# Performance work log

Measured on AMD Instinct MI355X. Metric: run time of the kernel, lower is better.

The kernel has to match this reference:

```python
import jax, jax.numpy as jnp
import numpy as np

K = 5  # box-blur width along disparity axis

def _blur_disparity(x):
    # depthwise conv1d with ones(K)/K kernel, zero 'same' padding, along axis 1
    N, D, H, W = x.shape
    xp = jnp.pad(x, ((0, 0), (K // 2, K // 2), (0, 0), (0, 0)))
    acc = xp[:, 0:D]
    for s in range(1, K):
        acc = acc + xp[:, s:s + D]
    return acc / K

def _modal_mask(x):
    N, D, H, W = x.shape
    index = jnp.argmax(x, axis=1, keepdims=True)                 # [N,1,H,W] int
    d = jnp.arange(D, dtype=x.dtype).reshape(1, D, 1, 1)
    d2 = jnp.arange(D + 1, dtype=x.dtype).reshape(1, D + 1, 1, 1)
    ones = jnp.ones((N, 1, H, W), dtype=x.dtype)
    x_diff_r = jnp.diff(x, axis=1, prepend=ones, append=ones)    # [N,D+1,H,W]
    x_diff_l = jnp.diff(x, axis=1, prepend=ones)                 # [N,D,H,W]
    # right edge of dominant mode: first positive diff strictly right of peak
    ind_r = ((x_diff_r * (d2 > index)) > 0).astype(jnp.int32)
    index_r = jnp.argmax(ind_r, axis=1, keepdims=True) - 1
    # left edge: last negative diff at/left of peak
    ind_l = ((x_diff_l * (d <= index)) < 0).astype(jnp.int32)
    index_l = D - 1 - jnp.argmax(jnp.flip(ind_l, axis=1), axis=1, keepdims=True)
    mask1 = (d >= index_l) & (d <= index_r)
    r = jnp.minimum(index_r - index, index - index_l)
    mask2 = (d >= index - r) & (d <= index + r)
    valid = jnp.abs(2 * index - index_r - index_l) < 3           # near-symmetric mode
    return jnp.where(valid, mask1, mask2)                        # bool [N,D,H,W]

def setup_inputs() -> dict:
    key = jax.random.key(0)
    N, D, H, W = 2, 192, 256, 512
    x = jax.random.uniform(key, (N, D, H, W), dtype=jnp.float32)
    return {"x": x}

def reference(x) -> jnp.ndarray:
    N, D, H, W = x.shape
    disp = jnp.arange(D, dtype=x.dtype).reshape(1, D, 1, 1)
    x_blur = _blur_disparity(x)
    mask = _modal_mask(x_blur)
    y = x * mask                       # primary mode mass
    z = x - y
    x_blur2 = x_blur * (~mask)
    z = z * _modal_mask(x_blur2)       # secondary mode mass
    valid = (jnp.sum(y, axis=1) >= jnp.sum(z, axis=1)).astype(jnp.float32)[:, None]
    xm = valid * y + (1.0 - valid) * z
    xm = xm / jnp.sum(xm, axis=1, keepdims=True)
    out = jnp.sum(xm * disp, axis=1, keepdims=True)  # [N,1,H,W]
    return out
```

## Files before the change

kernel.cpp:

```cpp
#include <hip/hip_runtime.h>
#include <math.h>

namespace {
constexpr int D     = 192;
constexpr int HW    = 256 * 512;
constexpr int TOTAL = 2 * HW;

__device__ __forceinline__ float div5(float s) {
    const float c = 0.2f;
    float q = s * c;
    float r = __builtin_fmaf(-5.0f, q, s);
    return __builtin_fmaf(r, c, q);
}

__device__ __forceinline__ bool in_range(int d, int lo, unsigned width) {
    return (unsigned)(d - lo) <= width;
}

struct Machine {
    float bprev, maxv;
    int   index, last_fall, index_l, index_r;
    bool  r_found;

    __device__ __forceinline__ void init() {
        bprev = 1.0f;
        maxv  = -INFINITY;
        index = 0; last_fall = 0; index_l = 0;
        index_r = D - 1;
        r_found = false;
    }

    __device__ __forceinline__ void step(int d, float b) {
        float diff = b - bprev;
        bool fall  = diff < 0.0f;
        last_fall  = fall ? d : last_fall;
        bool am    = b > maxv;
        maxv       = am ? b : maxv;
        index      = am ? d : index;
        index_l    = am ? last_fall : index_l;
        bool rise  = (diff > 0.0f) & (!r_found) & (!am);
        index_r    = am ? (D - 1) : (rise ? (d - 1) : index_r);
        r_found    = am ? false : (r_found | rise);
        bprev      = b;
    }

    __device__ __forceinline__ void finish(int& lo, unsigned& wd) const {
        int r = min(index_r - index, index - index_l);
        int t = 2 * index - index_r - index_l;
        bool valid = (t > -3) && (t < 3);
        lo = valid ? index_l : (index - r);
        int hi = valid ? index_r : (index + r);
        wd = (unsigned)(hi - lo);
    }
};

template<int OFS>
__device__ __forceinline__ void loadc(const float* __restrict__ col, int c,
                                      float (&buf)[8]) {
    #pragma unroll
    for (int j = 0; j < 8; ++j)
        buf[j] = col[(size_t)(8 * c + OFS + j) * HW];
}
template<int OFS>
__device__ __forceinline__ void loadc_guard(const float* __restrict__ col, int c,
                                            float (&buf)[8]) {
    #pragma unroll
    for (int j = 0; j < 8; ++j) {
        int idx = 8 * c + OFS + j;
        buf[j] = (idx < D) ? col[(size_t)idx * HW] : 0.0f;
    }
}

template<int OFS, typename F>
__device__ __forceinline__ void stream24(const float* __restrict__ col, F&& f) {
    float A[8], B[8], C[8];
    loadc<OFS>(col, 0, A);
    loadc<OFS>(col, 1, B);
    loadc<OFS>(col, 2, C);
    int d = 0;
    auto comp = [&](float (&buf)[8]) {
        #pragma unroll
        for (int j = 0; j < 8; ++j) { f(d, buf[j]); ++d; }
    };
    for (int g = 0; g < 6; ++g) {
        comp(A); loadc<OFS>(col, 3 * g + 3, A);
        comp(B); loadc<OFS>(col, 3 * g + 4, B);
        comp(C); loadc<OFS>(col, 3 * g + 5, C);
    }
    comp(A); loadc<OFS>(col, 21, A);
    comp(B); loadc<OFS>(col, 22, B);
    comp(C);
    if (OFS == 2) loadc_guard<OFS>(col, 23, C);
    else          loadc<OFS>(col, 23, C);
    comp(A); comp(B); comp(C);
}
}

extern "C" __global__ void __launch_bounds__(256, 4)
dme_kernel(const float* __restrict__ x, float* __restrict__ out)
{
    const int n  = blockIdx.x >> 9;
    const int hw = ((blockIdx.x & 511) << 8) | threadIdx.x;
    const float* __restrict__ col = x + (size_t)n * (size_t)(D * HW) + hw;

    const float x0 = col[0];
    const float x1 = col[HW];

    Machine m1; m1.init();
    {
        float w0 = 0.f, w1 = 0.f, w2 = x0, w3 = x1;
        stream24<2>(col, [&](int d, float xv) {
            float s = w0 + w1; s += w2; s += w3; s += xv;
            m1.step(d, div5(s));
            w0 = w1; w1 = w2; w2 = w3; w3 = xv;
        });
    }
    int lo1; unsigned wd1; m1.finish(lo1, wd1);

    Machine m2; m2.init();
    float sum_y = 0.f, wsum_y = 0.f;
    {
        float w0 = 0.f, w1 = 0.f, w2 = x0, w3 = x1;
        float fd = 0.0f;
        stream24<2>(col, [&](int d, float xv) {
            float s = w0 + w1; s += w2; s += w3; s += xv;
            float b = div5(s);
            bool in1 = in_range(d, lo1, wd1);
            m2.step(d, in1 ? 0.0f : b);
            sum_y += in1 ? w2 : 0.f;
            float t = in1 ? fd : 0.f;
            wsum_y = __builtin_fmaf(t, w2, wsum_y);
            w0 = w1; w1 = w2; w2 = w3; w3 = xv; fd += 1.0f;
        });
    }
    int lo2; unsigned wd2; m2.finish(lo2, wd2);

    float sum_z = 0.f, wsum_z = 0.f;
    {
        float fd = 0.0f;
        stream24<0>(col, [&](int d, float xv) {
            bool z = in_range(d, lo2, wd2) & !in_range(d, lo1, wd1);
            sum_z += z ? xv : 0.f;
            float t = z ? fd : 0.f;
            wsum_z = __builtin_fmaf(t, xv, wsum_z);
            fd += 1.0f;
        });
    }

    bool  v = (sum_y >= sum_z);
    float S = v ? sum_y  : sum_z;
    float W = v ? wsum_y : wsum_z;
    out[hw + n * HW] = W / S;
}

extern "C" void kernel_launch(void* const* d_in, const int* in_sizes, int n_in,
                              void* d_out, int out_size, void* d_ws, size_t ws_size,
                              hipStream_t stream)
{
    const float* x   = (const float*)d_in[0];
    float*       out = (float*)d_out;
    dim3 block(256), grid(TOTAL / 256);
    hipLaunchKernelGGL(dme_kernel, grid, block, 0, stream, x, out);
}
```

Measured before the change: 325.0 us.

## Load each disparity column into registers once and reuse across all passes

Instead of streaming the 192-element column from global memory three times, each thread loads the whole column into a 192-entry register array up front. The blur, both modal-mask passes and the final y/z accumulation then read from registers. This removes two of the three global reads per pixel. Launch bounds drop to 2 blocks per CU to leave room for the register file, and an empty asm barrier stops the compiler from keeping the blur sums alive across passes. The costs are lower occupancy and a risk of register spilling.

```diff
diff --git a/kernel.cpp b/kernel.cpp
--- a/kernel.cpp
+++ b/kernel.cpp
@@ -11,6 +11,11 @@
     float q = s * c;
     float r = __builtin_fmaf(-5.0f, q, s);
     return __builtin_fmaf(r, c, q);
+}
+
+__device__ __forceinline__ float opaque(float v) {
+    asm("" : "+v"(v));
+    return v;
 }
 
 __device__ __forceinline__ bool in_range(int d, int lo, unsigned width) {
@@ -53,98 +58,54 @@
         wd = (unsigned)(hi - lo);
     }
 };
-
-template<int OFS>
-__device__ __forceinline__ void loadc(const float* __restrict__ col, int c,
-                                      float (&buf)[8]) {
-    #pragma unroll
-    for (int j = 0; j < 8; ++j)
-        buf[j] = col[(size_t)(8 * c + OFS + j) * HW];
-}
-template<int OFS>
-__device__ __forceinline__ void loadc_guard(const float* __restrict__ col, int c,
-                                            float (&buf)[8]) {
-    #pragma unroll
-    for (int j = 0; j < 8; ++j) {
-        int idx = 8 * c + OFS + j;
-        buf[j] = (idx < D) ? col[(size_t)idx * HW] : 0.0f;
-    }
 }
 
-template<int OFS, typename F>
-__device__ __forceinline__ void stream24(const float* __restrict__ col, F&& f) {
-    float A[8], B[8], C[8];
-    loadc<OFS>(col, 0, A);
-    loadc<OFS>(col, 1, B);
-    loadc<OFS>(col, 2, C);
-    int d = 0;
-    auto comp = [&](float (&buf)[8]) {
-        #pragma unroll
-        for (int j = 0; j < 8; ++j) { f(d, buf[j]); ++d; }
-    };
-    for (int g = 0; g < 6; ++g) {
-        comp(A); loadc<OFS>(col, 3 * g + 3, A);
-        comp(B); loadc<OFS>(col, 3 * g + 4, B);
-        comp(C); loadc<OFS>(col, 3 * g + 5, C);
-    }
-    comp(A); loadc<OFS>(col, 21, A);
-    comp(B); loadc<OFS>(col, 22, B);
-    comp(C);
-    if (OFS == 2) loadc_guard<OFS>(col, 23, C);
-    else          loadc<OFS>(col, 23, C);
-    comp(A); comp(B); comp(C);
-}
-}
-
-extern "C" __global__ void __launch_bounds__(256, 4)
+extern "C" __global__ void __launch_bounds__(256, 2)
 dme_kernel(const float* __restrict__ x, float* __restrict__ out)
 {
     const int n  = blockIdx.x >> 9;
     const int hw = ((blockIdx.x & 511) << 8) | threadIdx.x;
     const float* __restrict__ col = x + (size_t)n * (size_t)(D * HW) + hw;
 
-    const float x0 = col[0];
-    const float x1 = col[HW];
+    float xv[D];
+    #pragma unroll
+    for (int d = 0; d < D; ++d) xv[d] = col[(size_t)d * HW];
 
     Machine m1; m1.init();
-    {
-        float w0 = 0.f, w1 = 0.f, w2 = x0, w3 = x1;
-        stream24<2>(col, [&](int d, float xv) {
-            float s = w0 + w1; s += w2; s += w3; s += xv;
-            m1.step(d, div5(s));
-            w0 = w1; w1 = w2; w2 = w3; w3 = xv;
-        });
+    #pragma unroll
+    for (int d = 0; d < D; ++d) {
+        float s = (d >= 2 ? xv[d - 2] : 0.0f) + (d >= 1 ? xv[d - 1] : 0.0f);
+        s += xv[d];
+        s += (d + 1 < D ? xv[d + 1] : 0.0f);
+        s += (d + 2 < D ? xv[d + 2] : 0.0f);
+        m1.step(d, div5(s));
     }
     int lo1; unsigned wd1; m1.finish(lo1, wd1);
 
     Machine m2; m2.init();
-    float sum_y = 0.f, wsum_y = 0.f;
-    {
-        float w0 = 0.f, w1 = 0.f, w2 = x0, w3 = x1;
-        float fd = 0.0f;
-        stream24<2>(col, [&](int d, float xv) {
-            float s = w0 + w1; s += w2; s += w3; s += xv;
-            float b = div5(s);
-            bool in1 = in_range(d, lo1, wd1);
-            m2.step(d, in1 ? 0.0f : b);
-            sum_y += in1 ? w2 : 0.f;
-            float t = in1 ? fd : 0.f;
-            wsum_y = __builtin_fmaf(t, w2, wsum_y);
-            w0 = w1; w1 = w2; w2 = w3; w3 = xv; fd += 1.0f;
-        });
+    #pragma unroll
+    for (int d = 0; d < D; ++d) {
+        float s = opaque(d >= 2 ? xv[d - 2] : 0.0f) + (d >= 1 ? xv[d - 1] : 0.0f);
+        s += xv[d];
+        s += (d + 1 < D ? xv[d + 1] : 0.0f);
+        s += (d + 2 < D ? xv[d + 2] : 0.0f);
+        float b = div5(s);
+        bool in1 = in_range(d, lo1, wd1);
+        m2.step(d, in1 ? 0.0f : b);
     }
     int lo2; unsigned wd2; m2.finish(lo2, wd2);
 
-    float sum_z = 0.f, wsum_z = 0.f;
-    {
-        float fd = 0.0f;
-        stream24<0>(col, [&](int d, float xv) {
-            bool z = in_range(d, lo2, wd2) & !in_range(d, lo1, wd1);
-            sum_z += z ? xv : 0.f;
-            float t = z ? fd : 0.f;
-            wsum_z = __builtin_fmaf(t, xv, wsum_z);
-            fd += 1.0f;
-        });
+    float sum_y = 0.f, wsum_y = 0.f, sum_z = 0.f, wsum_z = 0.f;
+    #pragma unroll
+    for (int d = 0; d < D; ++d) {
+        bool in1 = in_range(d, lo1, wd1);
+        bool zin = in_range(d, lo2, wd2) & !in1;
+        float ty = in1 ? xv[d] : 0.0f;
+        float tz = zin ? xv[d] : 0.0f;
+        sum_y += ty;
+        wsum_y = __builtin_fmaf((float)d, ty, wsum_y);
+        sum_z += tz;
+        wsum_z = __builtin_fmaf((float)d, tz, wsum_z);
     }
 
     bool  v = (sum_y >= sum_z);
```

Result: slower. 1.079 ms (+232.1%).
